# Kernel tuning notes

Measured on AMD Instinct MI355X. Metric: run time of the kernel, lower is better.

The kernel has to match this reference:

```python
import jax, jax.numpy as jnp
import numpy as np

N, CIN, T, V = 16, 16, 512, 200
K, COUT, H = 3, 64, 64


def setup_inputs() -> dict:
    key = jax.random.key(0)
    ks = jax.random.split(key, 9)
    s = 0.05
    return {
        "x": jax.random.normal(ks[0], (N, CIN, T, V), jnp.float32),
        "A": jax.random.uniform(ks[1], (K, V, V), jnp.float32) / V,
        "W_gcn": jax.random.normal(ks[2], (K * COUT, CIN), jnp.float32) * s,
        "b_gcn": jnp.zeros((K * COUT,), jnp.float32),
        "W_ih": jax.random.normal(ks[3], (4 * H, COUT), jnp.float32) * s,
        "W_hh": jax.random.normal(ks[4], (4 * H, H), jnp.float32) * s,
        "b_ih": jnp.zeros((4 * H,), jnp.float32),
        "b_hh": jnp.zeros((4 * H,), jnp.float32),
        "W_fc": jax.random.normal(ks[5], (1, H), jnp.float32) * s,
        "b_fc": jnp.zeros((1,), jnp.float32),
    }


def reference(x, A, W_gcn, b_gcn, W_ih, W_hh, b_ih, b_hh, W_fc, b_fc):
    n, c, t, v = x.shape
    k = A.shape[0]
    cout = W_gcn.shape[0] // k
    # ConvTemporalGraphical: 1x1 conv -> (n, k*cout, t, v), reshape, adjacency einsum
    y = jnp.einsum('nctv,oc->notv', x, W_gcn) + b_gcn[None, :, None, None]
    y = y.reshape(n, k, cout, t, v)
    y = jnp.einsum('nkctv,kvw->nctw', y, A)  # (n, cout, t, v)
    # mean over node dim, residual=False -> res=0
    y = jnp.mean(y, axis=3)  # (n, cout, t)
    seq = jnp.transpose(y, (2, 0, 1))  # (t, n, cout) time-major for scan

    def step(carry, xt):
        h, ccell = carry
        gates = xt @ W_ih.T + b_ih + h @ W_hh.T + b_hh  # (n, 4H)
        i, f, g, o = jnp.split(gates, 4, axis=-1)  # torch LSTM gate order
        i = jax.nn.sigmoid(i)
        f = jax.nn.sigmoid(f)
        g = jnp.tanh(g)
        o = jax.nn.sigmoid(o)
        ccell = f * ccell + i * g
        h = o * jnp.tanh(ccell)
        return (h, ccell), None

    h0 = jnp.zeros((n, W_hh.shape[1]), x.dtype)
    (h_last, _), _ = jax.lax.scan(step, (h0, h0), seq)
    out = h_last @ W_fc.T + b_fc  # (n, 1)
    return (out, A)
```

## Files before the change

### kernel.cpp

```cpp
#include <hip/hip_runtime.h>
#include <math.h>

#define N_    16
#define CIN_  16
#define T_    512
#define V_    200
#define K_    3
#define COUT_ 64
#define H_    64
#define G_    256

#define WS_A  0
#define WS_SA 640
#define WS_XA 1024
#define WS_XW (WS_XA + N_ * T_ * K_ * CIN_)

__device__ __forceinline__ float readlane_f(float v, int lane) {
    return __int_as_float(__builtin_amdgcn_readlane(__float_as_int(v), lane));
}

__global__ __launch_bounds__(256) void prep_kernel(const float* __restrict__ A,
                                                   float* __restrict__ out,
                                                   float* __restrict__ ws) {
    int tid = blockIdx.x * blockDim.x + threadIdx.x;
    if (tid < K_ * V_ * V_) out[16 + tid] = A[tid];
    if (tid < K_ * V_) {
        const float* row = A + (long)tid * V_;
        float s = 0.f;
        for (int w = 0; w < V_; ++w) s += row[w];
        ws[WS_A + tid] = s * (1.0f / V_);
    }
}

__global__ void sa_kernel(float* __restrict__ ws) {
    int k = threadIdx.x;
    if (k < K_) {
        float s = 0.f;
        for (int v = 0; v < V_; ++v) s += ws[WS_A + k * V_ + v];
        ws[WS_SA + k] = s;
    }
}

__global__ __launch_bounds__(256) void xa_kernel(const float* __restrict__ x,
                                                 float* __restrict__ ws) {
    __shared__ float aS[K_ * V_];
    int tid = threadIdx.x;
    for (int i = tid; i < K_ * V_; i += 256) aS[i] = ws[WS_A + i];
    __syncthreads();

    int wave = tid >> 6, lane = tid & 63;
    int row = blockIdx.x * 4 + wave;
    const float* xr = x + (long)row * V_;

    float s0 = 0.f, s1 = 0.f, s2 = 0.f;
    for (int v = lane; v < V_; v += 64) {
        float xv = xr[v];
        s0 = fmaf(xv, aS[v], s0);
        s1 = fmaf(xv, aS[V_ + v], s1);
        s2 = fmaf(xv, aS[2 * V_ + v], s2);
    }
    #pragma unroll
    for (int m = 1; m < 64; m <<= 1) {
        s0 += __shfl_xor(s0, m);
        s1 += __shfl_xor(s1, m);
        s2 += __shfl_xor(s2, m);
    }
    if (lane == 0) {
        int t  = row % T_;
        int nc = row / T_;
        int ci = nc % CIN_;
        int n  = nc / CIN_;
        long base = (long)(n * T_ + t) * (K_ * CIN_);
        ws[WS_XA + base + 0 * CIN_ + ci] = s0;
        ws[WS_XA + base + 1 * CIN_ + ci] = s1;
        ws[WS_XA + base + 2 * CIN_ + ci] = s2;
    }
}

__global__ __launch_bounds__(256) void gates_pre_kernel(
    const float* __restrict__ W_gcn, const float* __restrict__ b_gcn,
    const float* __restrict__ W_ih, const float* __restrict__ b_ih,
    const float* __restrict__ b_hh, float* __restrict__ ws) {
    int nt = blockIdx.x;
    int t = nt % T_, n = nt / T_;
    __shared__ float xaS[K_ * CIN_];
    __shared__ float seqS[COUT_];
    int tid = threadIdx.x;
    if (tid < K_ * CIN_)
        xaS[tid] = ws[WS_XA + (long)(n * T_ + t) * (K_ * CIN_) + tid];
    __syncthreads();
    if (tid < COUT_) {
        float s = 0.f;
        #pragma unroll
        for (int k = 0; k < K_; ++k) {
            s = fmaf(b_gcn[k * COUT_ + tid], ws[WS_SA + k], s);
            const float* wrow = W_gcn + (long)(k * COUT_ + tid) * CIN_;
            #pragma unroll
            for (int ci = 0; ci < CIN_; ++ci)
                s = fmaf(wrow[ci], xaS[k * CIN_ + ci], s);
        }
        seqS[tid] = s;
    }
    __syncthreads();
    float g = b_ih[tid] + b_hh[tid];
    const float* wrow = W_ih + (long)tid * H_;
    #pragma unroll 8
    for (int c = 0; c < H_; ++c) g = fmaf(wrow[c], seqS[c], g);
    ws[WS_XW + (long)(t * N_ + n) * G_ + tid] = g;
}

__global__ __launch_bounds__(256) void lstm_kernel(
    const float* __restrict__ W_hh, const float* __restrict__ W_fc,
    const float* __restrict__ b_fc, const float* __restrict__ ws,
    float* __restrict__ out) {
    int n = blockIdx.x;
    int w = threadIdx.x >> 6;
    int lane = threadIdx.x & 63;

    float whh[H_];
    const float* wr = W_hh + (long)(w * H_ + lane) * H_;
    #pragma unroll
    for (int c = 0; c < H_; ++c) whh[c] = wr[c];

    __shared__ float gbuf[2][4][H_];

    float h = 0.f, ccell = 0.f;

    const float* xw = ws + WS_XW + (long)n * G_ + (w * H_ + lane);
    float x0 = xw[0];
    float x1 = xw[(long)N_ * G_];

    for (int t = 0; t < T_; ++t) {
        float gate = x0;
        x0 = x1;
        if (t + 2 < T_) x1 = xw[(long)(t + 2) * N_ * G_];

        float a0 = 0.f, a1 = 0.f, a2 = 0.f, a3 = 0.f;
        #pragma unroll
        for (int c4 = 0; c4 < H_ / 4; ++c4) {
            a0 = fmaf(whh[4 * c4 + 0], readlane_f(h, 4 * c4 + 0), a0);
            a1 = fmaf(whh[4 * c4 + 1], readlane_f(h, 4 * c4 + 1), a1);
            a2 = fmaf(whh[4 * c4 + 2], readlane_f(h, 4 * c4 + 2), a2);
            a3 = fmaf(whh[4 * c4 + 3], readlane_f(h, 4 * c4 + 3), a3);
        }
        gate += (a0 + a1) + (a2 + a3);

        int p = t & 1;
        gbuf[p][w][lane] = gate;
        __syncthreads();
        float iv = gbuf[p][0][lane];
        float fv = gbuf[p][1][lane];
        float gv = gbuf[p][2][lane];
        float ov = gbuf[p][3][lane];
        iv = 1.f / (1.f + __expf(-iv));
        fv = 1.f / (1.f + __expf(-fv));
        gv = tanhf(gv);
        ov = 1.f / (1.f + __expf(-ov));
        ccell = fv * ccell + iv * gv;
        h = ov * tanhf(ccell);
    }

    if (w == 0) {
        float p = h * W_fc[lane];
        #pragma unroll
        for (int m = 1; m < 64; m <<= 1) p += __shfl_xor(p, m);
        if (lane == 0) out[n] = p + b_fc[0];
    }
}

extern "C" void kernel_launch(void* const* d_in, const int* in_sizes, int n_in,
                              void* d_out, int out_size, void* d_ws, size_t ws_size,
                              hipStream_t stream) {
    const float* x     = (const float*)d_in[0];
    const float* A     = (const float*)d_in[1];
    const float* W_gcn = (const float*)d_in[2];
    const float* b_gcn = (const float*)d_in[3];
    const float* W_ih  = (const float*)d_in[4];
    const float* W_hh  = (const float*)d_in[5];
    const float* b_ih  = (const float*)d_in[6];
    const float* b_hh  = (const float*)d_in[7];
    const float* W_fc  = (const float*)d_in[8];
    const float* b_fc  = (const float*)d_in[9];
    float* out = (float*)d_out;
    float* ws  = (float*)d_ws;

    int copy_elems = K_ * V_ * V_;
    prep_kernel<<<(copy_elems + 255) / 256, 256, 0, stream>>>(A, out, ws);
    sa_kernel<<<1, 64, 0, stream>>>(ws);
    int rows = N_ * CIN_ * T_;
    xa_kernel<<<rows / 4, 256, 0, stream>>>(x, ws);
    gates_pre_kernel<<<N_ * T_, 256, 0, stream>>>(W_gcn, b_gcn, W_ih, b_ih, b_hh, ws);
    lstm_kernel<<<N_, 256, 0, stream>>>(W_hh, W_fc, b_fc, ws, out);
}
```

Baseline: 429.6 us.

## Broadcast LSTM hidden state via LDS and compute cell update in one wave

The recurrent matvec now reads the hidden state from shared memory as float4 instead of 64 readlane ops per step. Only wave 0 computes the gate nonlinearities and cell update, then writes h to LDS, which adds a second barrier per timestep. Sigmoid and tanh use rcp/exp approximations instead of divide and tanhf. The goal is a shorter serial per-step latency in the 512-step recurrence, at the cost of an extra sync and slightly lower accuracy.

After: 402.0 us. 1.07x faster.

```diff
diff --git a/kernel.cpp b/kernel.cpp
--- a/kernel.cpp
+++ b/kernel.cpp
@@ -15,8 +15,11 @@
 #define WS_XA 1024
 #define WS_XW (WS_XA + N_ * T_ * K_ * CIN_)
 
-__device__ __forceinline__ float readlane_f(float v, int lane) {
-    return __int_as_float(__builtin_amdgcn_readlane(__float_as_int(v), lane));
+__device__ __forceinline__ float fast_sig(float x) {
+    return __builtin_amdgcn_rcpf(1.f + __expf(-x));
+}
+__device__ __forceinline__ float fast_tanh(float x) {
+    return fmaf(-2.f, __builtin_amdgcn_rcpf(1.f + __expf(2.f * x)), 1.f);
 }
 
 __global__ __launch_bounds__(256) void prep_kernel(const float* __restrict__ A,
@@ -109,7 +112,7 @@
     ws[WS_XW + (long)(t * N_ + n) * G_ + tid] = g;
 }
 
-__global__ __launch_bounds__(256) void lstm_kernel(
+__global__ __launch_bounds__(256, 1) void lstm_kernel(
     const float* __restrict__ W_hh, const float* __restrict__ W_fc,
     const float* __restrict__ b_fc, const float* __restrict__ ws,
     float* __restrict__ out) {
@@ -122,9 +125,12 @@
     #pragma unroll
     for (int c = 0; c < H_; ++c) whh[c] = wr[c];
 
-    __shared__ float gbuf[2][4][H_];
-
-    float h = 0.f, ccell = 0.f;
+    __shared__ __align__(16) float hS[H_];
+    __shared__ float gbuf[4][H_];
+
+    if (threadIdx.x < H_) hS[threadIdx.x] = 0.f;
+    float ccell = 0.f, hlast = 0.f;
+    __syncthreads();
 
     const float* xw = ws + WS_XW + (long)n * G_ + (w * H_ + lane);
     float x0 = xw[0];
@@ -136,32 +142,33 @@
         if (t + 2 < T_) x1 = xw[(long)(t + 2) * N_ * G_];
 
         float a0 = 0.f, a1 = 0.f, a2 = 0.f, a3 = 0.f;
+        const float4* h4 = (const float4*)hS;
         #pragma unroll
         for (int c4 = 0; c4 < H_ / 4; ++c4) {
-            a0 = fmaf(whh[4 * c4 + 0], readlane_f(h, 4 * c4 + 0), a0);
-            a1 = fmaf(whh[4 * c4 + 1], readlane_f(h, 4 * c4 + 1), a1);
-            a2 = fmaf(whh[4 * c4 + 2], readlane_f(h, 4 * c4 + 2), a2);
-            a3 = fmaf(whh[4 * c4 + 3], readlane_f(h, 4 * c4 + 3), a3);
+            float4 hv = h4[c4];
+            a0 = fmaf(whh[4 * c4 + 0], hv.x, a0);
+            a1 = fmaf(whh[4 * c4 + 1], hv.y, a1);
+            a2 = fmaf(whh[4 * c4 + 2], hv.z, a2);
+            a3 = fmaf(whh[4 * c4 + 3], hv.w, a3);
         }
         gate += (a0 + a1) + (a2 + a3);
 
-        int p = t & 1;
-        gbuf[p][w][lane] = gate;
+        gbuf[w][lane] = gate;
         __syncthreads();
-        float iv = gbuf[p][0][lane];
-        float fv = gbuf[p][1][lane];
-        float gv = gbuf[p][2][lane];
-        float ov = gbuf[p][3][lane];
-        iv = 1.f / (1.f + __expf(-iv));
-        fv = 1.f / (1.f + __expf(-fv));
-        gv = tanhf(gv);
-        ov = 1.f / (1.f + __expf(-ov));
-        ccell = fv * ccell + iv * gv;
-        h = ov * tanhf(ccell);
+        if (w == 0) {
+            float iv = fast_sig(gate);
+            float fv = fast_sig(gbuf[1][lane]);
+            float gv = fast_tanh(gbuf[2][lane]);
+            float ov = fast_sig(gbuf[3][lane]);
+            ccell = fmaf(fv, ccell, iv * gv);
+            hlast = ov * fast_tanh(ccell);
+            hS[lane] = hlast;
+        }
+        __syncthreads();
     }
 
     if (w == 0) {
-        float p = h * W_fc[lane];
+        float p = hlast * W_fc[lane];
         #pragma unroll
         for (int m = 1; m < 64; m <<= 1) p += __shfl_xor(p, m);
         if (lane == 0) out[n] = p + b_fc[0];
```
